# Kernel tuning notes

Measured on AMD Instinct MI355X. Metric: run time of the kernel, lower is better.

## Reference

```python
import jax, jax.numpy as jnp
import numpy as np

N_TOKENS = 4096
NUM_IN = 512
OUTPUT_DIMS = [512, 512, 256]
TOTAL_OUT = sum(OUTPUT_DIMS)  # 1280
N_EXPERTS = 8
TOP_K = 2
TEBD_DIM = 64
NTYPES = 128


def setup_inputs() -> dict:
    key = jax.random.key(0)
    ks = jax.random.split(key, 6)
    x = jax.random.normal(ks[0], (N_TOKENS, NUM_IN), dtype=jnp.float32)
    type_embeddings = jax.random.normal(ks[1], (NTYPES, TEBD_DIM), dtype=jnp.float32)
    atom_types = jax.random.randint(ks[2], (N_TOKENS,), 0, NTYPES)
    # learned parameters
    gate_in_dim = NUM_IN + TEBD_DIM
    W_gate = jax.random.normal(ks[3], (gate_in_dim, N_EXPERTS), dtype=jnp.float32) / np.sqrt(gate_in_dim)
    W_exp = jax.random.normal(ks[4], (N_EXPERTS, NUM_IN, TOTAL_OUT), dtype=jnp.float32) / np.sqrt(NUM_IN)
    b_exp = jax.random.normal(ks[5], (N_EXPERTS, TOTAL_OUT), dtype=jnp.float32) * 0.01
    return {"x": x, "type_embeddings": type_embeddings, "atom_types": atom_types,
            "W_gate": W_gate, "W_exp": W_exp, "b_exp": b_exp}


def reference(x, type_embeddings, atom_types, W_gate, W_exp, b_exp):
    # --- gating: atom-type-conditioned router (tebd_dim > 0) ---
    tebd = type_embeddings[atom_types]                      # [N, T]
    gate_in = jnp.concatenate([x, tebd], axis=-1)           # [N, D+T]
    logits = gate_in @ W_gate                               # [N, E]
    top_v, top_i = jax.lax.top_k(logits, TOP_K)             # [N, k]
    probs = jax.nn.softmax(top_v, axis=-1)                  # renormalized over selected experts
    # dense sparse-gate matrix [N, E] (zeros for unselected experts)
    gates = jnp.sum(jax.nn.one_hot(top_i, N_EXPERTS, dtype=x.dtype) * probs[..., None], axis=1)
    # --- expert compute (grouped GEMM expressed densely) ---
    y_all = jnp.einsum('nd,edo->neo', x, W_exp) + b_exp     # [N, E, O]
    fused = jnp.einsum('ne,neo->no', gates, y_all)          # [N, TOTAL_OUT]
    # --- split fused output per head ---
    splits = np.cumsum(OUTPUT_DIMS)[:-1].tolist()
    return tuple(jnp.split(fused, splits, axis=-1))
```

## Files before the change

kernel.cpp:

```cpp
#include <hip/hip_runtime.h>
#include <hip/hip_bf16.h>
#include <cstdint>
#include <cmath>

#define NT 4096
#define DIN 512
#define DOUT 1280
#define NE 8
#define TDIM 64
#define MAXTILES 80
#define NB 10
#define GATE_BLOCKS (NT / 4)
#define CONVW_BLOCKS (20 * (DIN / 64) * NE)
#define S1ROWS 5120

typedef __attribute__((ext_vector_type(8))) short bhalf8;
typedef __attribute__((ext_vector_type(8))) unsigned short ushort8;
typedef __attribute__((ext_vector_type(4))) float f32x4;

__device__ __forceinline__ unsigned short f2bf(float f) {
    __hip_bfloat16 h = __float2bfloat16(f);
    return *reinterpret_cast<unsigned short*>(&h);
}
__device__ __forceinline__ float bf2f(unsigned short u) {
    unsigned int v = (unsigned int)u << 16;
    return *reinterpret_cast<float*>(&v);
}

__device__ __forceinline__ void glds16(const unsigned short* g, unsigned short* l) {
    __builtin_amdgcn_global_load_lds(
        (const __attribute__((address_space(1))) void*)g,
        (__attribute__((address_space(3))) void*)l, 16, 0, 0);
}

__global__ __launch_bounds__(256) void prep_kernel(
    const float* __restrict__ x, const float* __restrict__ temb,
    const int* __restrict__ atype, const float* __restrict__ Wg,
    const float* __restrict__ W,
    unsigned short* __restrict__ xb, unsigned short* __restrict__ WT,
    int* __restrict__ e0a, int* __restrict__ e1a,
    float* __restrict__ g0a, float* __restrict__ g1a)
{
    __shared__ unsigned short t[64 * 72];
    const int tid = threadIdx.x;

    if ((int)blockIdx.x < GATE_BLOCKS) {
        const int n = blockIdx.x * 4 + (tid >> 6);
        const int l = tid & 63;

        float acc[NE];
#pragma unroll
        for (int e = 0; e < NE; ++e) acc[e] = 0.f;

        const float* xr = x + (size_t)n * DIN;
#pragma unroll
        for (int i = 0; i < DIN / 64; ++i) {
            const int k = i * 64 + l;
            const float xv = xr[k];
            xb[(size_t)n * DIN + k] = f2bf(xv);
            const float* wr = Wg + (size_t)k * NE;
#pragma unroll
            for (int e = 0; e < NE; ++e) acc[e] = fmaf(xv, wr[e], acc[e]);
        }
        {
            const int tt = atype[n];
            const float tv = temb[(size_t)tt * TDIM + l];
            const float* wr = Wg + (size_t)(DIN + l) * NE;
#pragma unroll
            for (int e = 0; e < NE; ++e) acc[e] = fmaf(tv, wr[e], acc[e]);
        }
#pragma unroll
        for (int off = 32; off > 0; off >>= 1) {
#pragma unroll
            for (int e = 0; e < NE; ++e) acc[e] += __shfl_xor(acc[e], off, 64);
        }
        if (l == 0) {
            int e0 = 0; float v0 = acc[0];
#pragma unroll
            for (int e = 1; e < NE; ++e) if (acc[e] > v0) { v0 = acc[e]; e0 = e; }
            int e1 = -1; float v1 = -INFINITY;
#pragma unroll
            for (int e = 0; e < NE; ++e) {
                if (e == e0) continue;
                if (acc[e] > v1) { v1 = acc[e]; e1 = e; }
            }
            const float p1 = expf(v1 - v0);
            const float s  = 1.f + p1;
            e0a[n] = e0; e1a[n] = e1; g0a[n] = 1.f / s; g1a[n] = p1 / s;
        }
    } else {
        const int b  = blockIdx.x - GATE_BLOCKS;
        const int n0 = (b % 20) * 64;
        const int k0 = ((b / 20) % (DIN / 64)) * 64;
        const int e  = b / (20 * (DIN / 64));
        const int nl = tid & 63;
        const int kb = tid >> 6;
#pragma unroll
        for (int r = 0; r < 16; ++r) {
            const int kl = r * 4 + kb;
            t[nl * 72 + kl] = f2bf(W[((size_t)e * DIN + k0 + kl) * DOUT + n0 + nl]);
        }
        __syncthreads();
        const int nw = tid >> 2;
        const int kc = tid & 3;
        uint4* dst = reinterpret_cast<uint4*>(
            WT + ((size_t)e * DOUT + n0 + nw) * DIN + k0 + kc * 16);
        const uint4* src = reinterpret_cast<const uint4*>(&t[nw * 72 + kc * 16]);
        dst[0] = src[0];
        dst[1] = src[1];
    }
}

#define SORT_T 1024
__global__ __launch_bounds__(1024) void sort_kernel(
    const int* __restrict__ e0a, const int* __restrict__ e1a,
    const float* __restrict__ g0a, const float* __restrict__ g1a,
    int* __restrict__ perm, float* __restrict__ pgate,
    int* __restrict__ tile_group, int* __restrict__ ipos1,
    int* __restrict__ meta2)
{
    __shared__ int hist[16 * SORT_T];
    __shared__ int gtot[16], gbase[16];
    const int t = threadIdx.x;
    for (int i = t; i < MAXTILES * 128; i += SORT_T) { perm[i] = 0; pgate[i] = 0.f; }
#pragma unroll
    for (int g = 0; g < 16; ++g) hist[g * SORT_T + t] = 0;
    __syncthreads();

    const int nbase = t * 4;
    int keys[8];
#pragma unroll
    for (int i = 0; i < 4; ++i) {
        const int n = nbase + i;
        keys[2 * i]     = e0a[n];
        keys[2 * i + 1] = 8 + e1a[n];
    }
#pragma unroll
    for (int i = 0; i < 8; ++i) hist[keys[i] * SORT_T + t] += 1;
    __syncthreads();

    const int w = t >> 6, l = t & 63;
    {
        int running = 0;
        for (int c = 0; c < SORT_T / 64; ++c) {
            int v = hist[w * SORT_T + c * 64 + l];
            int inc = v;
#pragma unroll
            for (int d = 1; d < 64; d <<= 1) {
                int u = __shfl_up(inc, d, 64);
                if (l >= d) inc += u;
            }
            hist[w * SORT_T + c * 64 + l] = running + inc - v;
            running += __shfl(inc, 63, 64);
        }
        if (l == 0) gtot[w] = running;
    }
    __syncthreads();
    if (t == 0) {
        int s = 0;
#pragma unroll
        for (int g = 0; g < 16; ++g) {
            gbase[g] = s;
            const int ntg = (gtot[g] + 127) >> 7;
            for (int k = 0; k < ntg; ++k) tile_group[s / 128 + k] = g;
            s += ntg * 128;
        }
        meta2[0] = s / 128;
        meta2[1] = gbase[8];
    }
    __syncthreads();

#pragma unroll
    for (int i = 0; i < 4; ++i) {
        const int n = nbase + i;
        {
            const int k = keys[2 * i];
            const int pos = gbase[k] + hist[k * SORT_T + t]++;
            perm[pos] = n; pgate[pos] = g0a[n];
        }
        {
            const int k = keys[2 * i + 1];
            const int pos = gbase[k] + hist[k * SORT_T + t]++;
            perm[pos] = n; pgate[pos] = g1a[n];
            ipos1[n] = pos - gbase[8];
        }
    }
}

__device__ __forceinline__ int swz(int row, int chunk) {
    return row * 64 + ((chunk ^ (row & 7)) << 3);
}

__global__ __launch_bounds__(256, 4) void gemm_kernel(
    const unsigned short* __restrict__ Xb,
    const unsigned short* __restrict__ WT,
    const float* __restrict__ bexp,
    const int* __restrict__ perm, const float* __restrict__ pgate,
    const int* __restrict__ tile_group, const int* __restrict__ meta2,
    unsigned short* __restrict__ stage, float* __restrict__ out)
{
    constexpr int NWG = MAXTILES * NB, CPX = NWG / 8;
    const int gid = blockIdx.x;
    const int wid = (gid & 7) * CPX + (gid >> 3);
    const int tile = wid / NB, nb = wid % NB;
    if (tile >= meta2[0]) return;
    const int g  = tile_group[tile];
    const int e  = g & 7;
    const bool s1 = (g >= 8);
    const int n0 = nb * 128;
    const int ph = tile & 7;

    __shared__ unsigned short As[128 * 64];
    __shared__ unsigned short Bs[128 * 64];
    __shared__ int   toks[128];
    __shared__ float gts[128];

    const int tid = threadIdx.x;
    if (tid < 128) {
        toks[tid] = perm[tile * 128 + tid];
        gts[tid]  = pgate[tile * 128 + tid];
    }
    __syncthreads();

    const int l = tid & 63;
    const int w = tid >> 6;
    const int lrow = l >> 3;
    const int schk = (l & 7) ^ lrow;

    const unsigned short* asrc[4];
    unsigned short* aldsb[4];
#pragma unroll
    for (int i = 0; i < 4; ++i) {
        asrc[i]  = Xb + (size_t)toks[i * 32 + w * 8 + lrow] * DIN + schk * 8;
        aldsb[i] = &As[(i * 32 + w * 8) * 64];
    }
    const unsigned short* bsrc[4];
    unsigned short* bldsb[4];
#pragma unroll
    for (int j = 0; j < 4; ++j) {
        bsrc[j]  = WT + ((size_t)e * DOUT + n0 + j * 32 + w * 8 + lrow) * DIN + schk * 8;
        bldsb[j] = &Bs[(j * 32 + w * 8) * 64];
    }

    f32x4 acc[4][4];
#pragma unroll
    for (int a = 0; a < 4; ++a)
#pragma unroll
        for (int b = 0; b < 4; ++b) acc[a][b] = (f32x4){0.f, 0.f, 0.f, 0.f};

    const int wm = w >> 1, wn = w & 1;
    const int fr = l & 15;
    const int fh = l >> 4;

#pragma unroll
    for (int t = 0; t < DIN / 64; ++t) {
        const int k0 = ((t + ph) & 7) * 64;
        __syncthreads();
#pragma unroll
        for (int i = 0; i < 4; ++i) glds16(asrc[i] + k0, aldsb[i]);
#pragma unroll
        for (int j = 0; j < 4; ++j) glds16(bsrc[j] + k0, bldsb[j]);
        __syncthreads();
#pragma unroll
        for (int ks = 0; ks < 2; ++ks) {
            bhalf8 af[4], bff[4];
#pragma unroll
            for (int fm = 0; fm < 4; ++fm)
                af[fm] = *reinterpret_cast<const bhalf8*>(
                    &As[swz(wm * 64 + fm * 16 + fr, ks * 4 + fh)]);
#pragma unroll
            for (int fn = 0; fn < 4; ++fn)
                bff[fn] = *reinterpret_cast<const bhalf8*>(
                    &Bs[swz(wn * 64 + fn * 16 + fr, ks * 4 + fh)]);
#pragma unroll
            for (int fm = 0; fm < 4; ++fm)
#pragma unroll
                for (int fn = 0; fn < 4; ++fn)
                    acc[fm][fn] = __builtin_amdgcn_mfma_f32_16x16x32_bf16(
                        af[fm], bff[fn], acc[fm][fn], 0, 0, 0);
        }
    }

    const int lc = l & 15, lr = l >> 4;
    float bval[4];
#pragma unroll
    for (int fn = 0; fn < 4; ++fn)
        bval[fn] = bexp[(size_t)e * DOUT + n0 + wn * 64 + fn * 16 + lc];

    if (s1) {
        const int srow0 = tile * 128 - meta2[1];
#pragma unroll
        for (int fm = 0; fm < 4; ++fm) {
#pragma unroll
            for (int j = 0; j < 4; ++j) {
                const int row = wm * 64 + fm * 16 + lr * 4 + j;
                const float gg = gts[row];
                unsigned short* sp = stage + (size_t)(srow0 + row) * DOUT + n0 + wn * 64 + lc;
#pragma unroll
                for (int fn = 0; fn < 4; ++fn)
                    sp[fn * 16] = f2bf(gg * (acc[fm][fn][j] + bval[fn]));
            }
        }
    } else {
        size_t base; int width, cstart;
        if (n0 < 512)       { base = 0;                 width = 512; cstart = n0; }
        else if (n0 < 1024) { base = (size_t)NT * 512;  width = 512; cstart = n0 - 512; }
        else                { base = (size_t)NT * 1024; width = 256; cstart = n0 - 1024; }
        const int coloff = cstart + wn * 64 + lc;
#pragma unroll
        for (int fm = 0; fm < 4; ++fm) {
#pragma unroll
            for (int j = 0; j < 4; ++j) {
                const int row = wm * 64 + fm * 16 + lr * 4 + j;
                const float gg = gts[row];
                if (gg != 0.f) {
                    float* op = out + base + (size_t)toks[row] * width + coloff;
#pragma unroll
                    for (int fn = 0; fn < 4; ++fn)
                        op[fn * 16] = gg * (acc[fm][fn][j] + bval[fn]);
                }
            }
        }
    }
}

__global__ __launch_bounds__(256) void combine_kernel(
    const unsigned short* __restrict__ stage, const int* __restrict__ ipos1,
    float* __restrict__ out)
{
    const int n = blockIdx.x * 4 + (threadIdx.x >> 6);
    const int l = threadIdx.x & 63;
    const ushort8* srow = reinterpret_cast<const ushort8*>(
        stage + (size_t)ipos1[n] * DOUT);
#pragma unroll
    for (int c = l; c < DOUT / 8; c += 64) {
        const ushort8 v8 = srow[c];
        const int col0 = c * 8;
        float* p;
        if (col0 < 512)       p = out + (size_t)n * 512 + col0;
        else if (col0 < 1024) p = out + (size_t)NT * 512 + (size_t)n * 512 + (col0 - 512);
        else                  p = out + (size_t)NT * 1024 + (size_t)n * 256 + (col0 - 1024);
        f32x4* pv = reinterpret_cast<f32x4*>(p);
        f32x4 a0 = pv[0], a1 = pv[1];
#pragma unroll
        for (int j = 0; j < 4; ++j) a0[j] += bf2f(v8[j]);
#pragma unroll
        for (int j = 0; j < 4; ++j) a1[j] += bf2f(v8[4 + j]);
        pv[0] = a0; pv[1] = a1;
    }
}

extern "C" void kernel_launch(void* const* d_in, const int* in_sizes, int n_in,
                              void* d_out, int out_size, void* d_ws, size_t ws_size,
                              hipStream_t stream) {
    const float* x     = (const float*)d_in[0];
    const float* temb  = (const float*)d_in[1];
    const int*   atype = (const int*)d_in[2];
    const float* Wg    = (const float*)d_in[3];
    const float* Wexp  = (const float*)d_in[4];
    const float* bexp  = (const float*)d_in[5];
    float* out = (float*)d_out;
    char*  ws  = (char*)d_ws;

    unsigned short* xb = (unsigned short*)(ws);
    unsigned short* wt = (unsigned short*)(ws + (size_t)4194304);
    unsigned short* stage = (unsigned short*)(ws + (size_t)14680064);
    const size_t META = 14680064 + (size_t)S1ROWS * DOUT * 2;
    char* meta = ws + META;
    int*   e0a = (int*)(meta);
    int*   e1a = (int*)(meta + 16384);
    float* g0a = (float*)(meta + 32768);
    float* g1a = (float*)(meta + 49152);
    int*   perm       = (int*)(meta + 65536);
    float* pgate      = (float*)(meta + 106496);
    int*   tile_group = (int*)(meta + 147456);
    int*   ipos1      = (int*)(meta + 147968);
    int*   meta2      = (int*)(meta + 164352);

    prep_kernel<<<dim3(GATE_BLOCKS + CONVW_BLOCKS), dim3(256), 0, stream>>>(
        x, temb, atype, Wg, Wexp, xb, wt, e0a, e1a, g0a, g1a);
    sort_kernel<<<dim3(1), dim3(SORT_T), 0, stream>>>(
        e0a, e1a, g0a, g1a, perm, pgate, tile_group, ipos1, meta2);
    gemm_kernel<<<dim3(MAXTILES * NB), dim3(256), 0, stream>>>(
        xb, wt, bexp, perm, pgate, tile_group, meta2, stage, out);
    combine_kernel<<<dim3(NT / 4), dim3(256), 0, stream>>>(stage, ipos1, out);
}
```

Baseline: 62.04 us.

## Use single-wave 64x64 GEMM blocks with double-buffered async LDS staging

Each GEMM workgroup is now one 64-lane wave computing a 64x64 output tile, so there are four times as many workgroups. Global-to-LDS loads are double-buffered and ordered with explicit vmcnt/lgkmcnt waits instead of __syncthreads, so the next K slice loads while MFMAs run on the current one. The per-tile K-phase rotation is dropped. In exchange, reuse of A and B loads within a block falls (more global traffic per FLOP), and correctness now depends on the hand-written waitcnt ordering.

```diff
diff --git a/kernel.cpp b/kernel.cpp
--- a/kernel.cpp
+++ b/kernel.cpp
@@ -9,7 +9,6 @@
 #define NE 8
 #define TDIM 64
 #define MAXTILES 80
-#define NB 10
 #define GATE_BLOCKS (NT / 4)
 #define CONVW_BLOCKS (20 * (DIN / 64) * NE)
 #define S1ROWS 5120
@@ -191,7 +190,7 @@
     return row * 64 + ((chunk ^ (row & 7)) << 3);
 }
 
-__global__ __launch_bounds__(256, 4) void gemm_kernel(
+__global__ __launch_bounds__(64) void gemm_kernel(
     const unsigned short* __restrict__ Xb,
     const unsigned short* __restrict__ WT,
     const float* __restrict__ bexp,
@@ -199,48 +198,47 @@
     const int* __restrict__ tile_group, const int* __restrict__ meta2,
     unsigned short* __restrict__ stage, float* __restrict__ out)
 {
-    constexpr int NWG = MAXTILES * NB, CPX = NWG / 8;
+    constexpr int NWG = MAXTILES * 40, CPX = NWG / 8;
     const int gid = blockIdx.x;
     const int wid = (gid & 7) * CPX + (gid >> 3);
-    const int tile = wid / NB, nb = wid % NB;
+    const int tile = wid / 40;
+    const int rem  = wid % 40;
+    const int half = rem / 20;
+    const int nb   = rem % 20;
     if (tile >= meta2[0]) return;
     const int g  = tile_group[tile];
     const int e  = g & 7;
     const bool s1 = (g >= 8);
-    const int n0 = nb * 128;
-    const int ph = tile & 7;
-
-    __shared__ unsigned short As[128 * 64];
-    __shared__ unsigned short Bs[128 * 64];
-    __shared__ int   toks[128];
-    __shared__ float gts[128];
-
-    const int tid = threadIdx.x;
-    if (tid < 128) {
-        toks[tid] = perm[tile * 128 + tid];
-        gts[tid]  = pgate[tile * 128 + tid];
-    }
-    __syncthreads();
-
-    const int l = tid & 63;
-    const int w = tid >> 6;
+    const int n0 = nb * 64;
+    const int row0 = tile * 128 + half * 64;
+
+    __shared__ unsigned short As[2][64 * 64];
+    __shared__ unsigned short Bs[2][64 * 64];
+    __shared__ int   toksS[64];
+    __shared__ float gtsS[64];
+
+    const int l = threadIdx.x;
+    toksS[l] = perm[row0 + l];
+    gtsS[l]  = pgate[row0 + l];
+    __syncthreads();
+
     const int lrow = l >> 3;
     const int schk = (l & 7) ^ lrow;
 
-    const unsigned short* asrc[4];
-    unsigned short* aldsb[4];
-#pragma unroll
-    for (int i = 0; i < 4; ++i) {
-        asrc[i]  = Xb + (size_t)toks[i * 32 + w * 8 + lrow] * DIN + schk * 8;
-        aldsb[i] = &As[(i * 32 + w * 8) * 64];
-    }
-    const unsigned short* bsrc[4];
-    unsigned short* bldsb[4];
-#pragma unroll
-    for (int j = 0; j < 4; ++j) {
-        bsrc[j]  = WT + ((size_t)e * DOUT + n0 + j * 32 + w * 8 + lrow) * DIN + schk * 8;
-        bldsb[j] = &Bs[(j * 32 + w * 8) * 64];
-    }
+    const unsigned short* asrc[8];
+    const unsigned short* bsrc[8];
+#pragma unroll
+    for (int r = 0; r < 8; ++r) {
+        asrc[r] = Xb + (size_t)toksS[r * 8 + lrow] * DIN + schk * 8;
+        bsrc[r] = WT + ((size_t)e * DOUT + n0 + r * 8 + lrow) * DIN + schk * 8;
+    }
+
+    auto STAGE = [&](int b, int k0) {
+#pragma unroll
+        for (int r = 0; r < 8; ++r) glds16(asrc[r] + k0, &As[b][(r * 8) * 64]);
+#pragma unroll
+        for (int r = 0; r < 8; ++r) glds16(bsrc[r] + k0, &Bs[b][(r * 8) * 64]);
+    };
 
     f32x4 acc[4][4];
 #pragma unroll
@@ -248,30 +246,29 @@
 #pragma unroll
         for (int b = 0; b < 4; ++b) acc[a][b] = (f32x4){0.f, 0.f, 0.f, 0.f};
 
-    const int wm = w >> 1, wn = w & 1;
     const int fr = l & 15;
     const int fh = l >> 4;
 
+    STAGE(0, 0);
+    STAGE(1, 64);
+
 #pragma unroll
     for (int t = 0; t < DIN / 64; ++t) {
-        const int k0 = ((t + ph) & 7) * 64;
-        __syncthreads();
-#pragma unroll
-        for (int i = 0; i < 4; ++i) glds16(asrc[i] + k0, aldsb[i]);
-#pragma unroll
-        for (int j = 0; j < 4; ++j) glds16(bsrc[j] + k0, bldsb[j]);
-        __syncthreads();
+        const int cb = t & 1;
+        if (t < DIN / 64 - 1) asm volatile("s_waitcnt vmcnt(16)" ::: "memory");
+        else                  asm volatile("s_waitcnt vmcnt(0)"  ::: "memory");
+        __builtin_amdgcn_sched_barrier(0);
 #pragma unroll
         for (int ks = 0; ks < 2; ++ks) {
             bhalf8 af[4], bff[4];
 #pragma unroll
             for (int fm = 0; fm < 4; ++fm)
                 af[fm] = *reinterpret_cast<const bhalf8*>(
-                    &As[swz(wm * 64 + fm * 16 + fr, ks * 4 + fh)]);
+                    &As[cb][swz(fm * 16 + fr, ks * 4 + fh)]);
 #pragma unroll
             for (int fn = 0; fn < 4; ++fn)
                 bff[fn] = *reinterpret_cast<const bhalf8*>(
-                    &Bs[swz(wn * 64 + fn * 16 + fr, ks * 4 + fh)]);
+                    &Bs[cb][swz(fn * 16 + fr, ks * 4 + fh)]);
 #pragma unroll
             for (int fm = 0; fm < 4; ++fm)
 #pragma unroll
@@ -279,23 +276,26 @@
                     acc[fm][fn] = __builtin_amdgcn_mfma_f32_16x16x32_bf16(
                         af[fm], bff[fn], acc[fm][fn], 0, 0, 0);
         }
+        asm volatile("s_waitcnt lgkmcnt(0)" ::: "memory");
+        __builtin_amdgcn_sched_barrier(0);
+        if (t + 2 < DIN / 64) STAGE(cb, (t + 2) * 64);
     }
 
     const int lc = l & 15, lr = l >> 4;
     float bval[4];
 #pragma unroll
     for (int fn = 0; fn < 4; ++fn)
-        bval[fn] = bexp[(size_t)e * DOUT + n0 + wn * 64 + fn * 16 + lc];
+        bval[fn] = bexp[(size_t)e * DOUT + n0 + fn * 16 + lc];
 
     if (s1) {
-        const int srow0 = tile * 128 - meta2[1];
+        const int srow0 = row0 - meta2[1];
 #pragma unroll
         for (int fm = 0; fm < 4; ++fm) {
 #pragma unroll
             for (int j = 0; j < 4; ++j) {
-                const int row = wm * 64 + fm * 16 + lr * 4 + j;
-                const float gg = gts[row];
-                unsigned short* sp = stage + (size_t)(srow0 + row) * DOUT + n0 + wn * 64 + lc;
+                const int row = fm * 16 + lr * 4 + j;
+                const float gg = gtsS[row];
+                unsigned short* sp = stage + (size_t)(srow0 + row) * DOUT + n0 + lc;
 #pragma unroll
                 for (int fn = 0; fn < 4; ++fn)
                     sp[fn * 16] = f2bf(gg * (acc[fm][fn][j] + bval[fn]));
@@ -306,15 +306,15 @@
         if (n0 < 512)       { base = 0;                 width = 512; cstart = n0; }
         else if (n0 < 1024) { base = (size_t)NT * 512;  width = 512; cstart = n0 - 512; }
         else                { base = (size_t)NT * 1024; width = 256; cstart = n0 - 1024; }
-        const int coloff = cstart + wn * 64 + lc;
+        const int coloff = cstart + lc;
 #pragma unroll
         for (int fm = 0; fm < 4; ++fm) {
 #pragma unroll
             for (int j = 0; j < 4; ++j) {
-                const int row = wm * 64 + fm * 16 + lr * 4 + j;
-                const float gg = gts[row];
+                const int row = fm * 16 + lr * 4 + j;
+                const float gg = gtsS[row];
                 if (gg != 0.f) {
-                    float* op = out + base + (size_t)toks[row] * width + coloff;
+                    float* op = out + base + (size_t)toksS[row] * width + coloff;
 #pragma unroll
                     for (int fn = 0; fn < 4; ++fn)
                         op[fn * 16] = gg * (acc[fm][fn][j] + bval[fn]);
@@ -381,7 +381,7 @@
         x, temb, atype, Wg, Wexp, xb, wt, e0a, e1a, g0a, g1a);
     sort_kernel<<<dim3(1), dim3(SORT_T), 0, stream>>>(
         e0a, e1a, g0a, g1a, perm, pgate, tile_group, ipos1, meta2);
-    gemm_kernel<<<dim3(MAXTILES * NB), dim3(256), 0, stream>>>(
+    gemm_kernel<<<dim3(MAXTILES * 40), dim3(64), 0, stream>>>(
         xb, wt, bexp, perm, pgate, tile_group, meta2, stage, out);
     combine_kernel<<<dim3(NT / 4), dim3(256), 0, stream>>>(stage, ipos1, out);
 }
```

Measured after the change: 75.39 us. 1.22x slower.
